# Optimization experiments

Measured on AMD Instinct MI355X. Metric: run time of the kernel, lower is better.

Reference implementation:

```python
import jax, jax.numpy as jnp
import numpy as np

S, LC = 4096, 16
N_WORD, N_CHAR = 100000, 128
CHAR_DIM, CHAR_HIDDEN = 64, 128
N_DIM, N_HIDDEN, N_TAG = 256, 512, 64


def setup_inputs() -> dict:
    key = jax.random.key(0)
    ks = jax.random.split(key, 16)
    rn = lambda k, shape, s=0.1: (jax.random.normal(k, shape, jnp.float32) * s)
    inp = {
        'char_emb': rn(ks[0], (N_CHAR, CHAR_DIM), 1.0),
        'char_Wih': rn(ks[1], (4 * CHAR_HIDDEN, CHAR_DIM)),
        'char_Whh': rn(ks[2], (4 * CHAR_HIDDEN, CHAR_HIDDEN)),
        'char_bih': rn(ks[3], (4 * CHAR_HIDDEN,)),
        'char_bhh': rn(ks[4], (4 * CHAR_HIDDEN,)),
        'word_emb': rn(ks[5], (N_WORD, N_DIM), 1.0),
        'Wih': rn(ks[6], (4 * N_HIDDEN, N_DIM + CHAR_HIDDEN)),
        'Whh': rn(ks[7], (4 * N_HIDDEN, N_HIDDEN)),
        'bih': rn(ks[8], (4 * N_HIDDEN,)),
        'bhh': rn(ks[9], (4 * N_HIDDEN,)),
        'W1': rn(ks[10], (N_TAG, N_HIDDEN)),
        'b1': rn(ks[11], (N_TAG,)),
        'x': jax.random.randint(ks[12], (S,), 0, N_WORD),
        'chars': jax.random.randint(ks[13], (S, LC), 0, N_CHAR),
        'char_lens': jax.random.randint(ks[14], (S,), 1, LC + 1),
    }
    return inp


def _lstm(xs, mask, Wih, Whh, bih, bhh):
    # xs: [T, B, In], mask: [T, B] bool. PyTorch gate order: i, f, g, o.
    T, B, _ = xs.shape
    H = Whh.shape[1]
    def step(carry, inp):
        h, c = carry
        x_t, m_t = inp
        g = x_t @ Wih.T + bih + h @ Whh.T + bhh  # [B, 4H]
        i, f, gg, o = jnp.split(g, 4, axis=-1)
        c_new = jax.nn.sigmoid(f) * c + jax.nn.sigmoid(i) * jnp.tanh(gg)
        h_new = jax.nn.sigmoid(o) * jnp.tanh(c_new)
        m = m_t[:, None]
        h2 = jnp.where(m, h_new, h)
        c2 = jnp.where(m, c_new, c)
        return (h2, c2), h2
    init = (jnp.zeros((B, H), xs.dtype), jnp.zeros((B, H), xs.dtype))
    (h_fin, _), hs = jax.lax.scan(step, init, (xs, mask))
    return hs, h_fin


def reference(char_emb, char_Wih, char_Whh, char_bih, char_bhh,
              word_emb, Wih, Whh, bih, bhh, W1, b1,
              x, chars, char_lens):
    # --- char-level LSTM, all S words batched (replaces per-word Python loop) ---
    cx = char_emb[chars]                      # [S, LC, char_dim]
    cx = jnp.transpose(cx, (1, 0, 2))         # [LC, S, char_dim]
    cmask = jnp.arange(LC)[:, None] < char_lens[None, :]  # [LC, S]
    _, char_h = _lstm(cx, cmask, char_Wih, char_Whh, char_bih, char_bhh)  # [S, char_hidden]

    # --- word-level LSTM over the sentence (batch 1, as in original) ---
    wx = word_emb[x]                          # [S, n_dim]
    feat = jnp.concatenate([wx, char_h], axis=-1)[:, None, :]  # [S, 1, n_dim+char_hidden]
    wmask = jnp.ones((feat.shape[0], 1), bool)
    hs, _ = _lstm(feat, wmask, Wih, Whh, bih, bhh)  # [S, 1, n_hidden]
    hs = hs[:, 0, :]

    logits = hs @ W1.T + b1                   # [S, n_tag]
    return jax.nn.log_softmax(logits, axis=-1)
```

## Files before the change

### kernel.cpp

```cpp
#include <hip/hip_runtime.h>
#include <hip/hip_bf16.h>
#include <hip/hip_fp16.h>


#define OFF_FLAG  0
#define OFF_CEMB  16
#define OFF_CWIH  8208
#define OFF_CBIH  40976
#define OFF_CBHH  41488
#define OFF_CWHH  42000
#define OFF_BIH   107536
#define OFF_BHH   109584
#define OFF_W1T   111632
#define OFF_CGE   144400
#define OFF_CH    209936
#define OFF_XP2   734224
#define OFF_HH    4928528
#define OFF_WHH16 5977104

#define SENT 0xFFFFFFFFu

#ifndef __has_builtin
#define __has_builtin(x) 0
#endif
#if __has_builtin(__builtin_amdgcn_fdot2)
#define HASDOT2 1
#endif

typedef _Float16 v2h __attribute__((ext_vector_type(2)));

__device__ __forceinline__ float sigf(float x) { return 1.0f / (1.0f + __expf(-x)); }
__device__ __forceinline__ float tanh_f(float x) { return 2.0f * sigf(2.0f * x) - 1.0f; }
__device__ __forceinline__ float b2f_lo(unsigned u) { return __uint_as_float(u << 16); }
__device__ __forceinline__ float b2f_hi(unsigned u) { return __uint_as_float(u & 0xFFFF0000u); }
__device__ __forceinline__ float h2f_lo(unsigned u) {
    union { unsigned short s; _Float16 h; } c;
    c.s = (unsigned short)(u & 0xFFFFu);
    return (float)c.h;
}
__device__ __forceinline__ float h2f_hi(unsigned u) {
    union { unsigned short s; _Float16 h; } c;
    c.s = (unsigned short)(u >> 16);
    return (float)c.h;
}
__device__ __forceinline__ unsigned short f2h_bits(float f) {
    union { unsigned short s; _Float16 h; } c;
    c.h = (_Float16)f;
    return c.s;
}
__device__ __forceinline__ float dot2h(unsigned w, unsigned h, float acc) {
#ifdef HASDOT2
    union U { unsigned u; v2h v; };
    U uw; uw.u = w;
    U uh; uh.u = h;
    return __builtin_amdgcn_fdot2(uw.v, uh.v, acc, false);
#else
    return acc + h2f_lo(w) * h2f_lo(h) + h2f_hi(w) * h2f_hi(h);
#endif
}

__global__ void detect_kernel(const unsigned* __restrict__ w, int* __restrict__ flagp) {
    unsigned v = w[threadIdx.x];
    unsigned e = (v >> 7) & 0xFF;
    int inr = (e >= 100 && e <= 140) ? 1 : 0;
    unsigned long long m = __ballot(inr);
    if (threadIdx.x == 0) flagp[0] = (__popcll(m) >= 56) ? 1 : 0;
}

__global__ void convf_kernel(const void* __restrict__ s, float* __restrict__ d,
                             int n, const int* __restrict__ flagp) {
    int i = blockIdx.x * 256 + threadIdx.x;
    if (i >= n) return;
    d[i] = flagp[0] ? __bfloat162float(((const __hip_bfloat16*)s)[i])
                    : ((const float*)s)[i];
}

__global__ void w1t_kernel(const void* __restrict__ W1, float* __restrict__ W1T,
                           const int* __restrict__ flagp) {
    int i = blockIdx.x * 256 + threadIdx.x;
    int j = i & 63, k = i >> 6;
    W1T[i] = flagp[0] ? __bfloat162float(((const __hip_bfloat16*)W1)[j * 512 + k])
                      : ((const float*)W1)[j * 512 + k];
}

__global__ void whh16_kernel(const void* __restrict__ src, unsigned short* __restrict__ dst,
                             const int* __restrict__ flagp) {
    int i = blockIdx.x * 256 + threadIdx.x;
    float f = flagp[0] ? __bfloat162float(((const __hip_bfloat16*)src)[i])
                       : ((const float*)src)[i];
    dst[i] = f2h_bits(f);
}

__global__ void __launch_bounds__(256) cge_kernel(
    const float* __restrict__ cemb, const float* __restrict__ cWih,
    const float* __restrict__ cbih, const float* __restrict__ cbhh,
    float* __restrict__ cge)
{
    __shared__ float xe[64];
    int c = blockIdx.x, tid = threadIdx.x;
    if (tid < 64) xe[tid] = cemb[c * 64 + tid];
    __syncthreads();
#pragma unroll
    for (int rep = 0; rep < 2; ++rep) {
        int j = rep * 256 + tid;
        float acc = cbih[j] + cbhh[j];
#pragma unroll 8
        for (int k = 0; k < 64; ++k)
            acc += xe[k] * cWih[j * 64 + k];
        cge[c * 512 + j] = acc;
    }
}

__global__ void __launch_bounds__(256) char_lstm_kernel(
    const float* __restrict__ cge, const float* __restrict__ Whh,
    const int* __restrict__ chars, const int* __restrict__ lens,
    float* __restrict__ char_h)
{
    __shared__ float hls[16][128];
    int tid = threadIdx.x;
    int wl = tid >> 4, sl = tid & 15;
    int w = blockIdx.x * 16 + wl;
    int len = lens[w];
    const int* cw = chars + w * 16;
    float c[8];
#pragma unroll
    for (int q = 0; q < 8; ++q) { c[q] = 0.0f; hls[wl][sl * 8 + q] = 0.0f; }

    for (int t = 0; t < 16; ++t) {
        __syncthreads();
        int ch = cw[t];
        const float* xg = cge + ch * 512;
        float acc[4][8];
#pragma unroll
        for (int g = 0; g < 4; ++g)
#pragma unroll
            for (int q = 0; q < 8; ++q)
                acc[g][q] = xg[g * 128 + sl * 8 + q];

        const float4* h4 = (const float4*)hls[wl];
#pragma unroll
        for (int g = 0; g < 4; ++g) {
            const float4* wbase = ((const float4*)Whh) + (g * 128 + sl * 8) * 32;
            for (int k4 = 0; k4 < 32; ++k4) {
                float4 hv = h4[k4];
#pragma unroll
                for (int q = 0; q < 8; ++q) {
                    float4 wv = wbase[q * 32 + k4];
                    acc[g][q] += wv.x * hv.x + wv.y * hv.y + wv.z * hv.z + wv.w * hv.w;
                }
            }
        }
        __syncthreads();
        if (t < len) {
#pragma unroll
            for (int q = 0; q < 8; ++q) {
                float iv = sigf(acc[0][q]);
                float fv = sigf(acc[1][q]);
                float gv = tanh_f(acc[2][q]);
                float ov = sigf(acc[3][q]);
                c[q] = fv * c[q] + iv * gv;
                hls[wl][sl * 8 + q] = ov * tanh_f(c[q]);
            }
        }
    }
    __syncthreads();
#pragma unroll
    for (int q = 0; q < 8; ++q)
        char_h[w * 128 + sl * 8 + q] = hls[wl][sl * 8 + q];
}

__global__ void __launch_bounds__(256) xp2_kernel(
    const void* __restrict__ wemb, const int* __restrict__ x,
    const float* __restrict__ char_h, const void* __restrict__ Wraw,
    const float* __restrict__ bih, const float* __restrict__ bhh,
    __hip_bfloat16* __restrict__ xp2, const int* __restrict__ flagp)
{
    __shared__ float feat[16][384];
    int flag = flagp[0];
    int tid = threadIdx.x, tl = tid >> 4, sl = tid & 15;
    int t = blockIdx.x * 16 + tl;
    int xw = x[t];
    for (int idx = sl; idx < 384; idx += 16) {
        float v;
        if (idx < 256)
            v = flag ? __bfloat162float(((const __hip_bfloat16*)wemb)[(size_t)xw * 256 + idx])
                     : ((const float*)wemb)[(size_t)xw * 256 + idx];
        else
            v = char_h[t * 128 + (idx - 256)];
        feat[tl][idx] = v;
    }
    __syncthreads();

    const float4* f4 = (const float4*)feat[tl];
    for (int rb = 0; rb < 4; ++rb) {
        int r0 = rb * 512 + sl * 32;
        for (int qc = 0; qc < 4; ++qc) {
            int rr = r0 + qc * 8;
            float acc[8];
#pragma unroll
            for (int q = 0; q < 8; ++q)
                acc[q] = bih[rr + q] + bhh[rr + q];
            if (!flag) {
                const float4* wb = ((const float4*)Wraw) + (size_t)rr * 96;
                for (int k4 = 0; k4 < 96; ++k4) {
                    float4 fv = f4[k4];
#pragma unroll
                    for (int q = 0; q < 8; ++q) {
                        float4 wv = wb[q * 96 + k4];
                        acc[q] += wv.x * fv.x + wv.y * fv.y + wv.z * fv.z + wv.w * fv.w;
                    }
                }
            } else {
                const uint2* wb = ((const uint2*)Wraw) + (size_t)rr * 96;
                for (int k4 = 0; k4 < 96; ++k4) {
                    float4 fv = f4[k4];
#pragma unroll
                    for (int q = 0; q < 8; ++q) {
                        uint2 wv = wb[q * 96 + k4];
                        acc[q] += b2f_lo(wv.x) * fv.x + b2f_hi(wv.x) * fv.y
                                + b2f_lo(wv.y) * fv.z + b2f_hi(wv.y) * fv.w;
                    }
                }
            }
#pragma unroll
            for (int q = 0; q < 8; ++q)
                xp2[(size_t)t * 2048 + rr + q] = __float2bfloat16(acc[q]);
        }
    }
}

__global__ void __launch_bounds__(1024, 1) word_lstm_kernel(
    const __hip_bfloat16* __restrict__ xp2, const unsigned* __restrict__ whh16,
    unsigned* __restrict__ hview)
{
    __shared__ __align__(16) unsigned hbufA[16][160];
    __shared__ __align__(16) unsigned hbufB[16][160];
    __shared__ float hout[2][32];
    int wg = blockIdx.x;
    int tid = threadIdx.x;
    int wave = tid >> 6, lane = tid & 63;
    int sp = lane >> 5;
    int g  = (lane >> 3) & 3;
    int kk = lane & 7;
    int slot = wg * 32 + wave * 2 + sp;
    int grow = g * 512 + slot;

    const uint4* wr = (const uint4*)(whh16 + (size_t)grow * 256) + kk * 8;
    uint4 wa0 = wr[0], wa1 = wr[1], wa2 = wr[2], wa3 = wr[3];
    uint4 wa4 = wr[4], wa5 = wr[5], wa6 = wr[6], wa7 = wr[7];

    const unsigned short* xpr = (const unsigned short*)xp2;
    unsigned* wbA = hbufA[wave];
    unsigned* wbB = hbufB[wave];
    unsigned* wdst = ((lane >> 4) & 1) ? wbB : wbA;
    int hj = (lane >> 4) >> 1;
    float c = 0.0f;
    int dead = 0;

#define PINU4(a) asm volatile("" : "+v"(a.x), "+v"(a.y), "+v"(a.z), "+v"(a.w))
    for (int t = 0; t < 4096; ++t) {
        unsigned short xraw = xpr[(size_t)t * 2048 + grow];
        PINU4(wa0); PINU4(wa1); PINU4(wa2); PINU4(wa3);
        PINU4(wa4); PINU4(wa5); PINU4(wa6); PINU4(wa7);

        if (t == 0) {
#pragma unroll
            for (int i = 0; i < 4; ++i)
                wdst[(hj + 2 * i) * 20 + (lane & 15)] = 0u;
        } else {
            const unsigned* src = hview + (size_t)(t - 1) * 256 + lane;
            unsigned v[4];
            unsigned spins = 0;
            for (;;) {
#pragma unroll
                for (int i = 0; i < 4; ++i)
                    v[i] = __hip_atomic_load(src + i * 64, __ATOMIC_RELAXED,
                                             __HIP_MEMORY_SCOPE_AGENT);
                int ok = 1;
#pragma unroll
                for (int i = 0; i < 4; ++i) ok &= (v[i] != SENT);
                if (dead || __all(ok)) break;
                if (++spins > (1u << 22)) { dead = 1; break; }
            }
            if (dead) {
#pragma unroll
                for (int i = 0; i < 4; ++i)
                    if (v[i] == SENT) v[i] = 0x3C003C00u;
            }
#pragma unroll
            for (int i = 0; i < 4; ++i)
                wdst[(hj + 2 * i) * 20 + (lane & 15)] = v[i];
        }

        const uint4* q0 = (const uint4*)(wbA + kk * 20);
        const uint4* q1 = (const uint4*)(wbB + kk * 20);
        float a0 = 0.0f, a1 = 0.0f, a2 = 0.0f, a3 = 0.0f;
        uint4 h4;
        h4 = q0[0]; a0 = dot2h(wa0.x, h4.x, a0); a1 = dot2h(wa0.y, h4.y, a1);
                    a2 = dot2h(wa0.z, h4.z, a2); a3 = dot2h(wa0.w, h4.w, a3);
        h4 = q0[1]; a0 = dot2h(wa1.x, h4.x, a0); a1 = dot2h(wa1.y, h4.y, a1);
                    a2 = dot2h(wa1.z, h4.z, a2); a3 = dot2h(wa1.w, h4.w, a3);
        h4 = q0[2]; a0 = dot2h(wa2.x, h4.x, a0); a1 = dot2h(wa2.y, h4.y, a1);
                    a2 = dot2h(wa2.z, h4.z, a2); a3 = dot2h(wa2.w, h4.w, a3);
        h4 = q0[3]; a0 = dot2h(wa3.x, h4.x, a0); a1 = dot2h(wa3.y, h4.y, a1);
                    a2 = dot2h(wa3.z, h4.z, a2); a3 = dot2h(wa3.w, h4.w, a3);
        h4 = q1[0]; a0 = dot2h(wa4.x, h4.x, a0); a1 = dot2h(wa4.y, h4.y, a1);
                    a2 = dot2h(wa4.z, h4.z, a2); a3 = dot2h(wa4.w, h4.w, a3);
        h4 = q1[1]; a0 = dot2h(wa5.x, h4.x, a0); a1 = dot2h(wa5.y, h4.y, a1);
                    a2 = dot2h(wa5.z, h4.z, a2); a3 = dot2h(wa5.w, h4.w, a3);
        h4 = q1[2]; a0 = dot2h(wa6.x, h4.x, a0); a1 = dot2h(wa6.y, h4.y, a1);
                    a2 = dot2h(wa6.z, h4.z, a2); a3 = dot2h(wa6.w, h4.w, a3);
        h4 = q1[3]; a0 = dot2h(wa7.x, h4.x, a0); a1 = dot2h(wa7.y, h4.y, a1);
                    a2 = dot2h(wa7.z, h4.z, a2); a3 = dot2h(wa7.w, h4.w, a3);
        float acc = (a0 + a1) + (a2 + a3);
        acc += __shfl_xor(acc, 1);
        acc += __shfl_xor(acc, 2);
        acc += __shfl_xor(acc, 4);
        float gvt = acc + __bfloat162float(*(const __hip_bfloat16*)&xraw);

        float iv = __shfl(gvt, sp * 32 + 0);
        float fv = __shfl(gvt, sp * 32 + 8);
        float gg = __shfl(gvt, sp * 32 + 16);
        float ov = __shfl(gvt, sp * 32 + 24);
        c = sigf(fv) * c + sigf(iv) * tanh_f(gg);
        float h = sigf(ov) * tanh_f(c);

        if ((lane & 31) == 0) hout[t & 1][wave * 2 + sp] = h;
        __syncthreads();

        if (wave == 0 && lane < 16) {
            unsigned u0 = f2h_bits(hout[t & 1][2 * lane]);
            unsigned u1 = f2h_bits(hout[t & 1][2 * lane + 1]);
            __hip_atomic_store(hview + (size_t)t * 256 + wg * 16 + lane,
                               u0 | (u1 << 16),
                               __ATOMIC_RELAXED, __HIP_MEMORY_SCOPE_AGENT);
        }
    }
#undef PINU4
}

__global__ void __launch_bounds__(64) out_kernel(
    const unsigned short* __restrict__ hh16, const float* __restrict__ W1T,
    const void* __restrict__ b1raw, void* __restrict__ out,
    const int* __restrict__ flagp)
{
    __shared__ float hb[512];
    int flag = flagp[0];
    int t = blockIdx.x, j = threadIdx.x;
    const unsigned* src = (const unsigned*)(hh16 + (size_t)t * 512);
#pragma unroll
    for (int kq = 0; kq < 4; ++kq) {
        unsigned u = src[j * 4 + kq];
        hb[j * 8 + 2 * kq]     = h2f_lo(u);
        hb[j * 8 + 2 * kq + 1] = h2f_hi(u);
    }
    __syncthreads();

    float acc = flag ? __bfloat162float(((const __hip_bfloat16*)b1raw)[j])
                     : ((const float*)b1raw)[j];
#pragma unroll 8
    for (int k = 0; k < 512; ++k)
        acc += hb[k] * W1T[k * 64 + j];

    float m = acc;
#pragma unroll
    for (int o = 32; o; o >>= 1) m = fmaxf(m, __shfl_xor(m, o));
    float e = __expf(acc - m);
    float s = e;
#pragma unroll
    for (int o = 32; o; o >>= 1) s += __shfl_xor(s, o);
    float r = acc - m - __logf(s);
    if (flag) ((__hip_bfloat16*)out)[t * 64 + j] = __float2bfloat16(r);
    else      ((float*)out)[t * 64 + j] = r;
}

extern "C" void kernel_launch(void* const* d_in, const int* in_sizes, int n_in,
                              void* d_out, int out_size, void* d_ws, size_t ws_size,
                              hipStream_t stream)
{
    (void)in_sizes; (void)n_in; (void)out_size; (void)ws_size;
    const void* char_emb = d_in[0];
    const void* char_Wih = d_in[1];
    const void* char_Whh = d_in[2];
    const void* char_bih = d_in[3];
    const void* char_bhh = d_in[4];
    const void* word_emb = d_in[5];
    const void* Wih      = d_in[6];
    const void* Whh      = d_in[7];
    const void* bih      = d_in[8];
    const void* bhh      = d_in[9];
    const void* W1       = d_in[10];
    const void* b1       = d_in[11];
    const int* x     = (const int*)d_in[12];
    const int* chars = (const int*)d_in[13];
    const int* lens  = (const int*)d_in[14];

    float* ws    = (float*)d_ws;
    int*   flagp = (int*)(ws + OFF_FLAG);
    float* cembf = ws + OFF_CEMB;
    float* cWihf = ws + OFF_CWIH;
    float* cbihf = ws + OFF_CBIH;
    float* cbhhf = ws + OFF_CBHH;
    float* cWhhf = ws + OFF_CWHH;
    float* bihf  = ws + OFF_BIH;
    float* bhhf  = ws + OFF_BHH;
    float* W1T   = ws + OFF_W1T;
    float* cge   = ws + OFF_CGE;
    float* charh = ws + OFF_CH;
    __hip_bfloat16* xp2 = (__hip_bfloat16*)(ws + OFF_XP2);
    unsigned short* hh16 = (unsigned short*)(ws + OFF_HH);
    unsigned short* whh16 = (unsigned short*)(ws + OFF_WHH16);

    (void)hipMemsetAsync(hh16, 0xFF, (size_t)4096 * 512 * 2, stream);

    detect_kernel<<<1, 64, 0, stream>>>((const unsigned*)char_emb, flagp);

    convf_kernel<<<(8192 + 255) / 256, 256, 0, stream>>>(char_emb, cembf, 8192, flagp);
    convf_kernel<<<(32768 + 255) / 256, 256, 0, stream>>>(char_Wih, cWihf, 32768, flagp);
    convf_kernel<<<2, 256, 0, stream>>>(char_bih, cbihf, 512, flagp);
    convf_kernel<<<2, 256, 0, stream>>>(char_bhh, cbhhf, 512, flagp);
    convf_kernel<<<(65536 + 255) / 256, 256, 0, stream>>>(char_Whh, cWhhf, 65536, flagp);
    convf_kernel<<<8, 256, 0, stream>>>(bih, bihf, 2048, flagp);
    convf_kernel<<<8, 256, 0, stream>>>(bhh, bhhf, 2048, flagp);
    w1t_kernel<<<128, 256, 0, stream>>>(W1, W1T, flagp);
    whh16_kernel<<<4096, 256, 0, stream>>>(Whh, whh16, flagp);

    cge_kernel<<<128, 256, 0, stream>>>(cembf, cWihf, cbihf, cbhhf, cge);
    char_lstm_kernel<<<256, 256, 0, stream>>>(cge, cWhhf, chars, lens, charh);
    xp2_kernel<<<256, 256, 0, stream>>>(word_emb, x, charh, Wih, bihf, bhhf, xp2, flagp);
    word_lstm_kernel<<<16, 1024, 0, stream>>>(xp2, (const unsigned*)whh16, (unsigned*)hh16);
    out_kernel<<<4096, 64, 0, stream>>>(hh16, W1T, b1, d_out, flagp);
}
```

Baseline: 12.75 ms.

## Halve word LSTM workgroups by giving each lane a double slice of Whh

The persistent word-level LSTM kernel now runs on 8 workgroups instead of 16. Each lane holds 16 uint4 of fp16 Whh in registers instead of 8, and 4 lanes reduce one gate row instead of 8, so each wave computes 4 hidden units. Fewer workgroups means fewer participants in the per-step cross-workgroup spin synchronization through global memory. In exchange, each lane does twice the dot-product work per step and register pressure rises. The asm register-pinning hints are also removed.

```diff
diff --git a/kernel.cpp b/kernel.cpp
--- a/kernel.cpp
+++ b/kernel.cpp
@@ -235,19 +235,21 @@
 {
     __shared__ __align__(16) unsigned hbufA[16][160];
     __shared__ __align__(16) unsigned hbufB[16][160];
-    __shared__ float hout[2][32];
+    __shared__ float hout[2][64];
     int wg = blockIdx.x;
     int tid = threadIdx.x;
     int wave = tid >> 6, lane = tid & 63;
-    int sp = lane >> 5;
-    int g  = (lane >> 3) & 3;
-    int kk = lane & 7;
-    int slot = wg * 32 + wave * 2 + sp;
+    int sp = lane >> 4;
+    int g  = (lane >> 2) & 3;
+    int kk = lane & 3;
+    int slot = wg * 64 + wave * 4 + sp;
     int grow = g * 512 + slot;
 
-    const uint4* wr = (const uint4*)(whh16 + (size_t)grow * 256) + kk * 8;
-    uint4 wa0 = wr[0], wa1 = wr[1], wa2 = wr[2], wa3 = wr[3];
-    uint4 wa4 = wr[4], wa5 = wr[5], wa6 = wr[6], wa7 = wr[7];
+    const uint4* wr = (const uint4*)(whh16 + (size_t)grow * 256) + kk * 16;
+    uint4 wa0  = wr[0],  wa1  = wr[1],  wa2  = wr[2],  wa3  = wr[3];
+    uint4 wa4  = wr[4],  wa5  = wr[5],  wa6  = wr[6],  wa7  = wr[7];
+    uint4 wa8  = wr[8],  wa9  = wr[9],  wa10 = wr[10], wa11 = wr[11];
+    uint4 wa12 = wr[12], wa13 = wr[13], wa14 = wr[14], wa15 = wr[15];
 
     const unsigned short* xpr = (const unsigned short*)xp2;
     unsigned* wbA = hbufA[wave];
@@ -257,11 +259,8 @@
     float c = 0.0f;
     int dead = 0;
 
-#define PINU4(a) asm volatile("" : "+v"(a.x), "+v"(a.y), "+v"(a.z), "+v"(a.w))
     for (int t = 0; t < 4096; ++t) {
         unsigned short xraw = xpr[(size_t)t * 2048 + grow];
-        PINU4(wa0); PINU4(wa1); PINU4(wa2); PINU4(wa3);
-        PINU4(wa4); PINU4(wa5); PINU4(wa6); PINU4(wa7);
 
         if (t == 0) {
 #pragma unroll
@@ -292,51 +291,69 @@
                 wdst[(hj + 2 * i) * 20 + (lane & 15)] = v[i];
         }
 
-        const uint4* q0 = (const uint4*)(wbA + kk * 20);
-        const uint4* q1 = (const uint4*)(wbB + kk * 20);
         float a0 = 0.0f, a1 = 0.0f, a2 = 0.0f, a3 = 0.0f;
         uint4 h4;
-        h4 = q0[0]; a0 = dot2h(wa0.x, h4.x, a0); a1 = dot2h(wa0.y, h4.y, a1);
-                    a2 = dot2h(wa0.z, h4.z, a2); a3 = dot2h(wa0.w, h4.w, a3);
-        h4 = q0[1]; a0 = dot2h(wa1.x, h4.x, a0); a1 = dot2h(wa1.y, h4.y, a1);
-                    a2 = dot2h(wa1.z, h4.z, a2); a3 = dot2h(wa1.w, h4.w, a3);
-        h4 = q0[2]; a0 = dot2h(wa2.x, h4.x, a0); a1 = dot2h(wa2.y, h4.y, a1);
-                    a2 = dot2h(wa2.z, h4.z, a2); a3 = dot2h(wa2.w, h4.w, a3);
-        h4 = q0[3]; a0 = dot2h(wa3.x, h4.x, a0); a1 = dot2h(wa3.y, h4.y, a1);
-                    a2 = dot2h(wa3.z, h4.z, a2); a3 = dot2h(wa3.w, h4.w, a3);
-        h4 = q1[0]; a0 = dot2h(wa4.x, h4.x, a0); a1 = dot2h(wa4.y, h4.y, a1);
-                    a2 = dot2h(wa4.z, h4.z, a2); a3 = dot2h(wa4.w, h4.w, a3);
-        h4 = q1[1]; a0 = dot2h(wa5.x, h4.x, a0); a1 = dot2h(wa5.y, h4.y, a1);
-                    a2 = dot2h(wa5.z, h4.z, a2); a3 = dot2h(wa5.w, h4.w, a3);
-        h4 = q1[2]; a0 = dot2h(wa6.x, h4.x, a0); a1 = dot2h(wa6.y, h4.y, a1);
-                    a2 = dot2h(wa6.z, h4.z, a2); a3 = dot2h(wa6.w, h4.w, a3);
-        h4 = q1[3]; a0 = dot2h(wa7.x, h4.x, a0); a1 = dot2h(wa7.y, h4.y, a1);
-                    a2 = dot2h(wa7.z, h4.z, a2); a3 = dot2h(wa7.w, h4.w, a3);
+        const uint4* q;
+        q = (const uint4*)(wbA + (2 * kk) * 20);
+        h4 = q[0]; a0 = dot2h(wa0.x, h4.x, a0); a1 = dot2h(wa0.y, h4.y, a1);
+                   a2 = dot2h(wa0.z, h4.z, a2); a3 = dot2h(wa0.w, h4.w, a3);
+        h4 = q[1]; a0 = dot2h(wa1.x, h4.x, a0); a1 = dot2h(wa1.y, h4.y, a1);
+                   a2 = dot2h(wa1.z, h4.z, a2); a3 = dot2h(wa1.w, h4.w, a3);
+        h4 = q[2]; a0 = dot2h(wa2.x, h4.x, a0); a1 = dot2h(wa2.y, h4.y, a1);
+                   a2 = dot2h(wa2.z, h4.z, a2); a3 = dot2h(wa2.w, h4.w, a3);
+        h4 = q[3]; a0 = dot2h(wa3.x, h4.x, a0); a1 = dot2h(wa3.y, h4.y, a1);
+                   a2 = dot2h(wa3.z, h4.z, a2); a3 = dot2h(wa3.w, h4.w, a3);
+        q = (const uint4*)(wbB + (2 * kk) * 20);
+        h4 = q[0]; a0 = dot2h(wa4.x, h4.x, a0); a1 = dot2h(wa4.y, h4.y, a1);
+                   a2 = dot2h(wa4.z, h4.z, a2); a3 = dot2h(wa4.w, h4.w, a3);
+        h4 = q[1]; a0 = dot2h(wa5.x, h4.x, a0); a1 = dot2h(wa5.y, h4.y, a1);
+                   a2 = dot2h(wa5.z, h4.z, a2); a3 = dot2h(wa5.w, h4.w, a3);
+        h4 = q[2]; a0 = dot2h(wa6.x, h4.x, a0); a1 = dot2h(wa6.y, h4.y, a1);
+                   a2 = dot2h(wa6.z, h4.z, a2); a3 = dot2h(wa6.w, h4.w, a3);
+        h4 = q[3]; a0 = dot2h(wa7.x, h4.x, a0); a1 = dot2h(wa7.y, h4.y, a1);
+                   a2 = dot2h(wa7.z, h4.z, a2); a3 = dot2h(wa7.w, h4.w, a3);
+        q = (const uint4*)(wbA + (2 * kk + 1) * 20);
+        h4 = q[0]; a0 = dot2h(wa8.x, h4.x, a0); a1 = dot2h(wa8.y, h4.y, a1);
+                   a2 = dot2h(wa8.z, h4.z, a2); a3 = dot2h(wa8.w, h4.w, a3);
+        h4 = q[1]; a0 = dot2h(wa9.x, h4.x, a0); a1 = dot2h(wa9.y, h4.y, a1);
+                   a2 = dot2h(wa9.z, h4.z, a2); a3 = dot2h(wa9.w, h4.w, a3);
+        h4 = q[2]; a0 = dot2h(wa10.x, h4.x, a0); a1 = dot2h(wa10.y, h4.y, a1);
+                   a2 = dot2h(wa10.z, h4.z, a2); a3 = dot2h(wa10.w, h4.w, a3);
+        h4 = q[3]; a0 = dot2h(wa11.x, h4.x, a0); a1 = dot2h(wa11.y, h4.y, a1);
+                   a2 = dot2h(wa11.z, h4.z, a2); a3 = dot2h(wa11.w, h4.w, a3);
+        q = (const uint4*)(wbB + (2 * kk + 1) * 20);
+        h4 = q[0]; a0 = dot2h(wa12.x, h4.x, a0); a1 = dot2h(wa12.y, h4.y, a1);
+                   a2 = dot2h(wa12.z, h4.z, a2); a3 = dot2h(wa12.w, h4.w, a3);
+        h4 = q[1]; a0 = dot2h(wa13.x, h4.x, a0); a1 = dot2h(wa13.y, h4.y, a1);
+                   a2 = dot2h(wa13.z, h4.z, a2); a3 = dot2h(wa13.w, h4.w, a3);
+        h4 = q[2]; a0 = dot2h(wa14.x, h4.x, a0); a1 = dot2h(wa14.y, h4.y, a1);
+                   a2 = dot2h(wa14.z, h4.z, a2); a3 = dot2h(wa14.w, h4.w, a3);
+        h4 = q[3]; a0 = dot2h(wa15.x, h4.x, a0); a1 = dot2h(wa15.y, h4.y, a1);
+                   a2 = dot2h(wa15.z, h4.z, a2); a3 = dot2h(wa15.w, h4.w, a3);
+
         float acc = (a0 + a1) + (a2 + a3);
         acc += __shfl_xor(acc, 1);
         acc += __shfl_xor(acc, 2);
-        acc += __shfl_xor(acc, 4);
         float gvt = acc + __bfloat162float(*(const __hip_bfloat16*)&xraw);
 
-        float iv = __shfl(gvt, sp * 32 + 0);
-        float fv = __shfl(gvt, sp * 32 + 8);
-        float gg = __shfl(gvt, sp * 32 + 16);
-        float ov = __shfl(gvt, sp * 32 + 24);
+        float iv = __shfl(gvt, sp * 16 + 0);
+        float fv = __shfl(gvt, sp * 16 + 4);
+        float gg = __shfl(gvt, sp * 16 + 8);
+        float ov = __shfl(gvt, sp * 16 + 12);
         c = sigf(fv) * c + sigf(iv) * tanh_f(gg);
         float h = sigf(ov) * tanh_f(c);
 
-        if ((lane & 31) == 0) hout[t & 1][wave * 2 + sp] = h;
+        if ((lane & 15) == 0) hout[t & 1][wave * 4 + sp] = h;
         __syncthreads();
 
-        if (wave == 0 && lane < 16) {
+        if (wave == 0 && lane < 32) {
             unsigned u0 = f2h_bits(hout[t & 1][2 * lane]);
             unsigned u1 = f2h_bits(hout[t & 1][2 * lane + 1]);
-            __hip_atomic_store(hview + (size_t)t * 256 + wg * 16 + lane,
+            __hip_atomic_store(hview + (size_t)t * 256 + wg * 32 + lane,
                                u0 | (u1 << 16),
                                __ATOMIC_RELAXED, __HIP_MEMORY_SCOPE_AGENT);
         }
     }
-#undef PINU4
 }
 
 __global__ void __launch_bounds__(64) out_kernel(
@@ -428,6 +445,6 @@
     cge_kernel<<<128, 256, 0, stream>>>(cembf, cWihf, cbihf, cbhhf, cge);
     char_lstm_kernel<<<256, 256, 0, stream>>>(cge, cWhhf, chars, lens, charh);
     xp2_kernel<<<256, 256, 0, stream>>>(word_emb, x, charh, Wih, bihf, bhhf, xp2, flagp);
-    word_lstm_kernel<<<16, 1024, 0, stream>>>(xp2, (const unsigned*)whh16, (unsigned*)hh16);
+    word_lstm_kernel<<<8, 1024, 0, stream>>>(xp2, (const unsigned*)whh16, (unsigned*)hh16);
     out_kernel<<<4096, 64, 0, stream>>>(hh16, W1T, b1, d_out, flagp);
 }
```

Result: slower. 13.27 ms (+4.0%).
